# Kernel optimization log

Measured on AMD Instinct MI355X. Metric: run time of the kernel, lower is better.

## Reference

```python
import jax, jax.numpy as jnp
import numpy as np

N_NODES = 100000
IN_F = 256
OUT_F = 128
N_EDGES = 1600000


def setup_inputs() -> dict:
    key = jax.random.key(0)
    k1, k2, k3, k4, k5 = jax.random.split(key, 5)
    x = jax.random.normal(k1, (N_NODES, IN_F), dtype=jnp.float32)
    edge_index = jax.random.randint(k2, (2, N_EDGES), 0, N_NODES, dtype=jnp.int64)
    edge_weight = jax.random.uniform(k3, (N_EDGES,), dtype=jnp.float32)
    # Xavier-uniform init as in reset_parameters
    limit = float(np.sqrt(6.0 / (IN_F + OUT_F)))
    weight = jax.random.uniform(k4, (IN_F, OUT_F), dtype=jnp.float32,
                                minval=-limit, maxval=limit)
    return {"x": x, "edge_index": edge_index, "edge_weight": edge_weight,
            "weight": weight}


def reference(x, edge_index, edge_weight, weight):
    # support = X @ W  -- dense feature transform
    support = x @ weight                       # [N, out_f]
    # output = spmm(adj, support): out[dst] += w_e * support[src]
    dst = edge_index[0]
    src = edge_index[1]
    msgs = support[src] * edge_weight[:, None]  # [E, out_f] gather
    out = jax.ops.segment_sum(msgs, dst, num_segments=N_NODES)  # [N, out_f]
    return out
```

## Files before the change

### kernel.cpp

```cpp
#include <hip/hip_runtime.h>

#define N_NODES 100000
#define IN_F 256
#define OUT_F 128
#define NB 782
#define LCAP 4096

typedef float f32x4 __attribute__((ext_vector_type(4)));
typedef __bf16 bf16x8 __attribute__((ext_vector_type(8)));

__device__ inline unsigned cvt2_bf16(float a, float b) {
  unsigned ua = __float_as_uint(a), ub = __float_as_uint(b);
  ua = (ua + 0x7fffu + ((ua >> 16) & 1u)) >> 16;
  ub = (ub + 0x7fffu + ((ub >> 16) & 1u)) >> 16;
  return ua | (ub << 16);
}
__device__ inline unsigned short cvt1_bf16(float a) {
  unsigned ua = __float_as_uint(a);
  return (unsigned short)((ua + 0x7fffu + ((ua >> 16) & 1u)) >> 16);
}

__global__ __launch_bounds__(256) void transpose_w(const float* __restrict__ w,
                                                   uint4* __restrict__ wt) {
  int c = blockIdx.x * 256 + threadIdx.x;
  int l = c & 63;
  int kt = (c >> 6) & 7;
  int nt = c >> 9;
  int n = nt * 16 + (l & 15);
  int kb = kt * 32 + ((l >> 4) & 3) * 8;
  unsigned d[4];
#pragma unroll
  for (int j = 0; j < 4; ++j) {
    float a = w[(size_t)(kb + 2 * j) * OUT_F + n];
    float b = w[(size_t)(kb + 2 * j + 1) * OUT_F + n];
    d[j] = cvt2_bf16(a, b);
  }
  wt[c] = make_uint4(d[0], d[1], d[2], d[3]);
}

__global__ __launch_bounds__(256) void gemm_count(const float* __restrict__ x,
                                                  const uint4* __restrict__ wt,
                                                  unsigned short* __restrict__ sup,
                                                  const int* __restrict__ ei,
                                                  int* __restrict__ coarse,
                                                  int nedges, int nblk, int gblocks) {
  __shared__ uint4 As[1024];
  __shared__ uint4 Bs[1024];
  __shared__ int hist[NB];
  const int gid = blockIdx.x;
  const int t = threadIdx.x;

  int role, sub;
  int m = (gblocks < nblk) ? gblocks : nblk;
  if (gid < 2 * m) {
    role = gid & 1;
    sub = gid >> 1;
  } else if (nblk > gblocks) {
    role = 1;
    sub = gid - gblocks;
  } else {
    role = 0;
    sub = gid - nblk;
  }

  if (role == 1) {
    for (int i = t; i < NB; i += 256) hist[i] = 0;
    __syncthreads();
    const int base = sub * 2048;
#pragma unroll
    for (int j = 0; j < 8; ++j) {
      int e = base + j * 256 + t;
      if (e < nedges) atomicAdd(&hist[ei[e] >> 7], 1);
    }
    __syncthreads();
    for (int i = t; i < NB; i += 256) coarse[(size_t)sub * NB + i] = hist[i];
    return;
  }

  const int lane = t & 63;
  const int wv = t >> 6;
  const int wm = wv >> 1, wn = wv & 1;
  const int row0 = sub * 128;

  f32x4 acc[4][4];
#pragma unroll
  for (int mi = 0; mi < 4; ++mi)
#pragma unroll
    for (int ni = 0; ni < 4; ++ni) acc[mi][ni] = (f32x4){0.f, 0.f, 0.f, 0.f};

  for (int it = 0; it < 4; ++it) {
    const int k0 = it * 64;
#pragma unroll
    for (int i = 0; i < 4; ++i) {
      int ci = i * 256 + t;
      int g = ci >> 6, l = ci & 63;
      int mrow = (g >> 1) * 16 + (l & 15);
      int k = k0 + (g & 1) * 32 + ((l >> 4) & 3) * 8;
      int row = row0 + mrow;
      if (row > N_NODES - 1) row = N_NODES - 1;
      const float* src = x + (size_t)row * IN_F + k;
      f32x4 v0 = *(const f32x4*)src;
      f32x4 v1 = *(const f32x4*)(src + 4);
      As[ci] = make_uint4(cvt2_bf16(v0.x, v0.y), cvt2_bf16(v0.z, v0.w),
                          cvt2_bf16(v1.x, v1.y), cvt2_bf16(v1.z, v1.w));
      Bs[ci] = wt[((g >> 1) * 8 + it * 2 + (g & 1)) * 64 + l];
    }
    __syncthreads();
#pragma unroll
    for (int ktl = 0; ktl < 2; ++ktl) {
      bf16x8 af[4], bfr[4];
#pragma unroll
      for (int mi = 0; mi < 4; ++mi)
        af[mi] = *(bf16x8*)&As[((wm * 4 + mi) * 2 + ktl) * 64 + lane];
#pragma unroll
      for (int ni = 0; ni < 4; ++ni)
        bfr[ni] = *(bf16x8*)&Bs[((wn * 4 + ni) * 2 + ktl) * 64 + lane];
#pragma unroll
      for (int mi = 0; mi < 4; ++mi)
#pragma unroll
        for (int ni = 0; ni < 4; ++ni)
          acc[mi][ni] = __builtin_amdgcn_mfma_f32_16x16x32_bf16(af[mi], bfr[ni],
                                                                acc[mi][ni], 0, 0, 0);
    }
    __syncthreads();
  }

  const int quad = lane >> 4, col = lane & 15;
#pragma unroll
  for (int mi = 0; mi < 4; ++mi) {
#pragma unroll
    for (int r = 0; r < 4; ++r) {
      int row = row0 + (wm * 4 + mi) * 16 + quad * 4 + r;
      if (row < N_NODES) {
#pragma unroll
        for (int ni = 0; ni < 4; ++ni)
          sup[(size_t)row * OUT_F + (wn * 4 + ni) * 16 + col] =
              cvt1_bf16(acc[mi][ni][r]);
      }
    }
  }
}

__global__ __launch_bounds__(256) void colscan(int* __restrict__ coarse,
                                               int* __restrict__ coltot, int nblk) {
  __shared__ int s[256];
  const int bin = blockIdx.x;
  const int t = threadIdx.x;
  int carry = 0;
  for (int c0 = 0; c0 < nblk; c0 += 256) {
    int idx = c0 + t;
    int v = (idx < nblk) ? coarse[(size_t)idx * NB + bin] : 0;
    s[t] = v;
    __syncthreads();
    for (int off = 1; off < 256; off <<= 1) {
      int xv = (t >= off) ? s[t - off] : 0;
      __syncthreads();
      s[t] += xv;
      __syncthreads();
    }
    int excl = carry + ((t == 0) ? 0 : s[t - 1]);
    if (idx < nblk) coarse[(size_t)idx * NB + bin] = excl;
    carry += s[255];
    __syncthreads();
  }
  if (t == 0) coltot[bin] = carry;
}

__global__ __launch_bounds__(256) void scan1(int* __restrict__ a,
                                             int* __restrict__ bsum, int n) {
  __shared__ int s[256];
  const int t = threadIdx.x;
  const int base = blockIdx.x * 1024 + t * 4;
  int v0 = (base + 0 < n) ? a[base + 0] : 0;
  int v1 = (base + 1 < n) ? a[base + 1] : 0;
  int v2 = (base + 2 < n) ? a[base + 2] : 0;
  int v3 = (base + 3 < n) ? a[base + 3] : 0;
  v1 += v0; v2 += v1; v3 += v2;
  s[t] = v3;
  __syncthreads();
  for (int off = 1; off < 256; off <<= 1) {
    int xv = (t >= off) ? s[t - off] : 0;
    __syncthreads();
    s[t] += xv;
    __syncthreads();
  }
  int excl = (t == 0) ? 0 : s[t - 1];
  if (base + 0 < n) a[base + 0] = v0 + excl;
  if (base + 1 < n) a[base + 1] = v1 + excl;
  if (base + 2 < n) a[base + 2] = v2 + excl;
  if (base + 3 < n) a[base + 3] = v3 + excl;
  if (t == 255 && bsum) bsum[blockIdx.x] = s[255];
}

__global__ __launch_bounds__(256) void partition(const int* __restrict__ ei,
                                                 const float* __restrict__ ew,
                                                 const int* __restrict__ coarse,
                                                 const int* __restrict__ coltot,
                                                 int2* __restrict__ recs, int nedges) {
  __shared__ int wbase[NB];
  const int b = blockIdx.x;
  const int t = threadIdx.x;
  for (int i = t; i < NB; i += 256)
    wbase[i] = coarse[(size_t)b * NB + i] + (i ? coltot[i - 1] : 0);
  __syncthreads();
  const int base = b * 2048;
#pragma unroll
  for (int j = 0; j < 8; ++j) {
    int e = base + j * 256 + t;
    if (e < nedges) {
      int d = ei[e];
      int srcn = ei[nedges + e];
      float wv = ew[e];
      int bin = d >> 7;
      int pos = atomicAdd(&wbase[bin], 1);
      unsigned long long pk =
          (unsigned long long)(unsigned)((srcn << 7) | (d & 127)) |
          ((unsigned long long)__float_as_uint(wv) << 32);
      __builtin_nontemporal_store(pk, (unsigned long long*)&recs[pos]);
    }
  }
}

__global__ __launch_bounds__(256) void fine_csr(int2* __restrict__ recs,
                                                const int* __restrict__ coltot,
                                                int* __restrict__ rowptr) {
  __shared__ int2 lrec[LCAP];
  __shared__ int cnt[128];
  __shared__ int wp[128];
  const int bin = blockIdx.x;
  const int t = threadIdx.x;
  const int segStart = bin ? coltot[bin - 1] : 0;
  const int segEnd = coltot[bin];
  int nrec = segEnd - segStart;
  if (nrec > LCAP) nrec = LCAP;
  if (t < 128) cnt[t] = 0;
  __syncthreads();
  for (int i = t; i < nrec; i += 256) {
    int2 r = recs[segStart + i];
    lrec[i] = r;
    atomicAdd(&cnt[r.x & 127], 1);
  }
  __syncthreads();
  for (int off = 1; off < 128; off <<= 1) {
    int xv = (t >= off && t < 128) ? cnt[t - off] : 0;
    __syncthreads();
    if (t < 128) cnt[t] += xv;
    __syncthreads();
  }
  if (t < 128) {
    wp[t] = segStart + ((t == 0) ? 0 : cnt[t - 1]);
    int node = bin * 128 + t;
    if (node < N_NODES) rowptr[node + 1] = segStart + cnt[t];
  }
  if (bin == 0 && t == 0) rowptr[0] = 0;
  __syncthreads();
  for (int i = t; i < nrec; i += 256) {
    int2 r = lrec[i];
    int p = atomicAdd(&wp[r.x & 127], 1);
    recs[p] = make_int2(r.x >> 7, r.y);
  }
}

__global__ __launch_bounds__(256) void aggregate_bf16(const int* __restrict__ rowptr,
                                                      const int2* __restrict__ edges,
                                                      const unsigned short* __restrict__ sup,
                                                      float* __restrict__ out, int nnodes) {
  int wave = (int)((blockIdx.x * 256u + threadIdx.x) >> 6);
  int lane = threadIdx.x & 63;
  if (wave >= nnodes) return;
  int beg = rowptr[wave];
  int end = rowptr[wave + 1];
  float2 acc = make_float2(0.f, 0.f);
  int e = beg;
  for (; e + 4 <= end; e += 4) {
    int2 m0 = edges[e + 0];
    int2 m1 = edges[e + 1];
    int2 m2 = edges[e + 2];
    int2 m3 = edges[e + 3];
    unsigned u0 = *(const unsigned*)(sup + (size_t)m0.x * OUT_F + lane * 2);
    unsigned u1 = *(const unsigned*)(sup + (size_t)m1.x * OUT_F + lane * 2);
    unsigned u2 = *(const unsigned*)(sup + (size_t)m2.x * OUT_F + lane * 2);
    unsigned u3 = *(const unsigned*)(sup + (size_t)m3.x * OUT_F + lane * 2);
    float w0 = __int_as_float(m0.y), w1 = __int_as_float(m1.y);
    float w2 = __int_as_float(m2.y), w3 = __int_as_float(m3.y);
    acc.x = fmaf(__uint_as_float(u0 << 16), w0, acc.x);
    acc.y = fmaf(__uint_as_float(u0 & 0xffff0000u), w0, acc.y);
    acc.x = fmaf(__uint_as_float(u1 << 16), w1, acc.x);
    acc.y = fmaf(__uint_as_float(u1 & 0xffff0000u), w1, acc.y);
    acc.x = fmaf(__uint_as_float(u2 << 16), w2, acc.x);
    acc.y = fmaf(__uint_as_float(u2 & 0xffff0000u), w2, acc.y);
    acc.x = fmaf(__uint_as_float(u3 << 16), w3, acc.x);
    acc.y = fmaf(__uint_as_float(u3 & 0xffff0000u), w3, acc.y);
  }
  for (; e < end; ++e) {
    int2 m = edges[e];
    unsigned u = *(const unsigned*)(sup + (size_t)m.x * OUT_F + lane * 2);
    float w = __int_as_float(m.y);
    acc.x = fmaf(__uint_as_float(u << 16), w, acc.x);
    acc.y = fmaf(__uint_as_float(u & 0xffff0000u), w, acc.y);
  }
  *(float2*)(out + (size_t)wave * OUT_F + lane * 2) = acc;
}

__global__ __launch_bounds__(256) void gemm_mfma(const float* __restrict__ x,
                                                 const uint4* __restrict__ wt,
                                                 unsigned short* __restrict__ sup) {
  __shared__ uint4 As[1024];
  __shared__ uint4 Bs[1024];
  const int t = threadIdx.x;
  const int lane = t & 63;
  const int wv = t >> 6;
  const int wm = wv >> 1, wn = wv & 1;
  const int row0 = blockIdx.x * 128;

  f32x4 acc[4][4];
#pragma unroll
  for (int mi = 0; mi < 4; ++mi)
#pragma unroll
    for (int ni = 0; ni < 4; ++ni) acc[mi][ni] = (f32x4){0.f, 0.f, 0.f, 0.f};

  for (int it = 0; it < 4; ++it) {
    const int k0 = it * 64;
#pragma unroll
    for (int i = 0; i < 4; ++i) {
      int ci = i * 256 + t;
      int g = ci >> 6, l = ci & 63;
      int m = (g >> 1) * 16 + (l & 15);
      int k = k0 + (g & 1) * 32 + ((l >> 4) & 3) * 8;
      int row = row0 + m;
      if (row > N_NODES - 1) row = N_NODES - 1;
      const float* src = x + (size_t)row * IN_F + k;
      f32x4 v0 = *(const f32x4*)src;
      f32x4 v1 = *(const f32x4*)(src + 4);
      As[ci] = make_uint4(cvt2_bf16(v0.x, v0.y), cvt2_bf16(v0.z, v0.w),
                          cvt2_bf16(v1.x, v1.y), cvt2_bf16(v1.z, v1.w));
      Bs[ci] = wt[((g >> 1) * 8 + it * 2 + (g & 1)) * 64 + l];
    }
    __syncthreads();
#pragma unroll
    for (int ktl = 0; ktl < 2; ++ktl) {
      bf16x8 af[4], bfr[4];
#pragma unroll
      for (int mi = 0; mi < 4; ++mi)
        af[mi] = *(bf16x8*)&As[((wm * 4 + mi) * 2 + ktl) * 64 + lane];
#pragma unroll
      for (int ni = 0; ni < 4; ++ni)
        bfr[ni] = *(bf16x8*)&Bs[((wn * 4 + ni) * 2 + ktl) * 64 + lane];
#pragma unroll
      for (int mi = 0; mi < 4; ++mi)
#pragma unroll
        for (int ni = 0; ni < 4; ++ni)
          acc[mi][ni] = __builtin_amdgcn_mfma_f32_16x16x32_bf16(af[mi], bfr[ni],
                                                                acc[mi][ni], 0, 0, 0);
    }
    __syncthreads();
  }

  const int quad = lane >> 4, col = lane & 15;
#pragma unroll
  for (int mi = 0; mi < 4; ++mi) {
#pragma unroll
    for (int r = 0; r < 4; ++r) {
      int row = row0 + (wm * 4 + mi) * 16 + quad * 4 + r;
      if (row < N_NODES) {
#pragma unroll
        for (int ni = 0; ni < 4; ++ni)
          sup[(size_t)row * OUT_F + (wn * 4 + ni) * 16 + col] =
              cvt1_bf16(acc[mi][ni][r]);
      }
    }
  }
}

__global__ __launch_bounds__(256) void scatter_edges(const int* __restrict__ ei,
                                                     const float* __restrict__ ew,
                                                     const unsigned short* __restrict__ sup,
                                                     float* __restrict__ out, int nedges) {
  int gwave = (int)((blockIdx.x * 256u + threadIdx.x) >> 6);
  int lane = threadIdx.x & 63;
  if (gwave >= nedges) return;
  int dst = ei[gwave];
  int src = ei[nedges + gwave];
  float wgt = ew[gwave];
  unsigned u = *(const unsigned*)(sup + (size_t)src * OUT_F + lane * 2);
  float* op = out + (size_t)dst * OUT_F + lane * 2;
  atomicAdd(op, __uint_as_float(u << 16) * wgt);
  atomicAdd(op + 1, __uint_as_float(u & 0xffff0000u) * wgt);
}

extern "C" void kernel_launch(void* const* d_in, const int* in_sizes, int n_in,
                              void* d_out, int out_size, void* d_ws, size_t ws_size,
                              hipStream_t stream) {
  const float* x = (const float*)d_in[0];
  const int* ei = (const int*)d_in[1];
  const float* ew = (const float*)d_in[2];
  const float* w = (const float*)d_in[3];
  float* out = (float*)d_out;
  const int nedges = in_sizes[2];
  const int nblk = (nedges + 2047) / 2048;

  const size_t off_support = 0;
  const size_t sz_support = (size_t)N_NODES * OUT_F * 2;
  const size_t off_rowptr = off_support + sz_support;
  const size_t off_wt = off_rowptr + 400016;
  const size_t off_coltot = off_wt + 65536;
  const size_t off_coarse = off_coltot + 3136;
  const size_t sz_coarse = (size_t)nblk * NB * 4;
  const size_t off_recs = (off_coarse + sz_coarse + 15) & ~(size_t)15;
  const size_t total_ws = off_recs + (size_t)nedges * 8;

  unsigned short* support = (unsigned short*)((char*)d_ws + off_support);
  int* rowptr = (int*)((char*)d_ws + off_rowptr);
  uint4* wt = (uint4*)((char*)d_ws + off_wt);
  int* coltot = (int*)((char*)d_ws + off_coltot);
  int* coarse = (int*)((char*)d_ws + off_coarse);
  int2* recs = (int2*)((char*)d_ws + off_recs);

  transpose_w<<<16, 256, 0, stream>>>(w, wt);

  if (ws_size < total_ws) {
    const int gblocks = (N_NODES + 127) / 128;
    gemm_mfma<<<gblocks, 256, 0, stream>>>(x, wt, support);
    hipMemsetAsync(d_out, 0, (size_t)out_size * sizeof(float), stream);
    int sblocks = (nedges + 3) / 4;
    scatter_edges<<<sblocks, 256, 0, stream>>>(ei, ew, support, out, nedges);
    return;
  }

  const int gblocks = (N_NODES + 127) / 128;

  gemm_count<<<gblocks + nblk, 256, 0, stream>>>(x, wt, support, ei, coarse,
                                                 nedges, nblk, gblocks);
  colscan<<<NB, 256, 0, stream>>>(coarse, coltot, nblk);
  scan1<<<1, 256, 0, stream>>>(coltot, (int*)nullptr, NB);
  partition<<<nblk, 256, 0, stream>>>(ei, ew, coarse, coltot, recs, nedges);
  fine_csr<<<NB, 256, 0, stream>>>(recs, coltot, rowptr);

  const int ablocks = (N_NODES + 3) / 4;
  aggregate_bf16<<<ablocks, 256, 0, stream>>>(rowptr, recs, support, out, N_NODES);
}
```

Baseline: 350.8 us.

## Sort edges locally per block during GEMM, merge bins in fine CSR pass

The counting blocks that run alongside the GEMM now do a full local counting sort of their 2048 edges by coarse bin in shared memory. They write the sorted records and 16-bit per-block bin offsets to a workspace buffer. The separate partition kernel and the strided column scan are replaced by a simple per-bin column sum. The fine CSR kernel now gathers each bin's runs from every block buffer and sorts them through an index array instead of re-reading scattered records. This removes one full pass over the edge list and the random global scatter, at the cost of many small, poorly coalesced gathers in fine_csr2 and a lower per-bin capacity (3072).

```diff
diff --git a/kernel.cpp b/kernel.cpp
--- a/kernel.cpp
+++ b/kernel.cpp
@@ -4,7 +4,8 @@
 #define IN_F 256
 #define OUT_F 128
 #define NB 782
-#define LCAP 4096
+#define EPB 2048
+#define LCAP2 3072
 
 typedef float f32x4 __attribute__((ext_vector_type(4)));
 typedef __bf16 bf16x8 __attribute__((ext_vector_type(8)));
@@ -38,15 +39,15 @@
   wt[c] = make_uint4(d[0], d[1], d[2], d[3]);
 }
 
-__global__ __launch_bounds__(256) void gemm_count(const float* __restrict__ x,
-                                                  const uint4* __restrict__ wt,
-                                                  unsigned short* __restrict__ sup,
-                                                  const int* __restrict__ ei,
-                                                  int* __restrict__ coarse,
-                                                  int nedges, int nblk, int gblocks) {
-  __shared__ uint4 As[1024];
-  __shared__ uint4 Bs[1024];
-  __shared__ int hist[NB];
+__global__ __launch_bounds__(256) void gemm_sort(const float* __restrict__ x,
+                                                 const uint4* __restrict__ wt,
+                                                 unsigned short* __restrict__ sup,
+                                                 const int* __restrict__ ei,
+                                                 const float* __restrict__ ew,
+                                                 unsigned short* __restrict__ lst,
+                                                 int2* __restrict__ buf1,
+                                                 int nedges, int nblk, int gblocks) {
+  __shared__ __align__(16) char smem[32768];
   const int gid = blockIdx.x;
   const int t = threadIdx.x;
 
@@ -64,19 +65,63 @@
   }
 
   if (role == 1) {
+    int2* ebuf = (int2*)smem;
+    int* hist = (int*)(smem + 16384);
+    int* scn = (int*)(smem + 19520);
+    int* tmp = (int*)(smem + 22656);
+    const int base = sub * EPB;
+    const int nE = min(EPB, nedges - base);
+
     for (int i = t; i < NB; i += 256) hist[i] = 0;
     __syncthreads();
-    const int base = sub * 2048;
+    int d8[8], ok8[8];
 #pragma unroll
     for (int j = 0; j < 8; ++j) {
       int e = base + j * 256 + t;
-      if (e < nedges) atomicAdd(&hist[ei[e] >> 7], 1);
-    }
-    __syncthreads();
-    for (int i = t; i < NB; i += 256) coarse[(size_t)sub * NB + i] = hist[i];
+      ok8[j] = e < nedges;
+      d8[j] = ok8[j] ? ei[e] : 0;
+      if (ok8[j]) atomicAdd(&hist[d8[j] >> 7], 1);
+    }
+    __syncthreads();
+    int carry = 0;
+    for (int c0 = 0; c0 < NB; c0 += 256) {
+      int idx = c0 + t;
+      int v = (idx < NB) ? hist[idx] : 0;
+      tmp[t] = v;
+      __syncthreads();
+      for (int off = 1; off < 256; off <<= 1) {
+        int xv = (t >= off) ? tmp[t - off] : 0;
+        __syncthreads();
+        tmp[t] += xv;
+        __syncthreads();
+      }
+      if (idx < NB) scn[idx] = carry + tmp[t] - v;
+      int nc = carry + tmp[255];
+      __syncthreads();
+      carry = nc;
+    }
+    for (int i = t; i < NB; i += 256)
+      lst[(size_t)sub * (NB + 2) + i] = (unsigned short)scn[i];
+    if (t == 0) lst[(size_t)sub * (NB + 2) + NB] = (unsigned short)nE;
+    for (int i = t; i < NB; i += 256) hist[i] = scn[i];
+    __syncthreads();
+#pragma unroll
+    for (int j = 0; j < 8; ++j) {
+      if (ok8[j]) {
+        int e = base + j * 256 + t;
+        int srcn = ei[nedges + e];
+        float wv = ew[e];
+        int pos = atomicAdd(&hist[d8[j] >> 7], 1);
+        ebuf[pos] = make_int2((srcn << 7) | (d8[j] & 127), __float_as_int(wv));
+      }
+    }
+    __syncthreads();
+    for (int i = t; i < nE; i += 256) buf1[(size_t)sub * EPB + i] = ebuf[i];
     return;
   }
 
+  uint4* As = (uint4*)smem;
+  uint4* Bs = (uint4*)(smem + 16384);
   const int lane = t & 63;
   const int wv = t >> 6;
   const int wm = wv >> 1, wn = wv & 1;
@@ -141,29 +186,17 @@
   }
 }
 
-__global__ __launch_bounds__(256) void colscan(int* __restrict__ coarse,
-                                               int* __restrict__ coltot, int nblk) {
-  __shared__ int s[256];
-  const int bin = blockIdx.x;
-  const int t = threadIdx.x;
-  int carry = 0;
-  for (int c0 = 0; c0 < nblk; c0 += 256) {
-    int idx = c0 + t;
-    int v = (idx < nblk) ? coarse[(size_t)idx * NB + bin] : 0;
-    s[t] = v;
-    __syncthreads();
-    for (int off = 1; off < 256; off <<= 1) {
-      int xv = (t >= off) ? s[t - off] : 0;
-      __syncthreads();
-      s[t] += xv;
-      __syncthreads();
-    }
-    int excl = carry + ((t == 0) ? 0 : s[t - 1]);
-    if (idx < nblk) coarse[(size_t)idx * NB + bin] = excl;
-    carry += s[255];
-    __syncthreads();
-  }
-  if (t == 0) coltot[bin] = carry;
+__global__ __launch_bounds__(256) void colsum(const unsigned short* __restrict__ lst,
+                                              int* __restrict__ coltot, int nblk) {
+  int bin = blockIdx.x * 256 + threadIdx.x;
+  if (bin >= NB) return;
+  int sum = 0;
+  for (int s = 0; s < nblk; ++s) {
+    int a = lst[(size_t)s * (NB + 2) + bin];
+    int b = lst[(size_t)s * (NB + 2) + bin + 1];
+    sum += b - a;
+  }
+  coltot[bin] = sum;
 }
 
 __global__ __launch_bounds__(256) void scan1(int* __restrict__ a,
@@ -192,54 +225,57 @@
   if (t == 255 && bsum) bsum[blockIdx.x] = s[255];
 }
 
-__global__ __launch_bounds__(256) void partition(const int* __restrict__ ei,
-                                                 const float* __restrict__ ew,
-                                                 const int* __restrict__ coarse,
+__global__ __launch_bounds__(256) void fine_csr2(const int2* __restrict__ buf1,
+                                                 const unsigned short* __restrict__ lst,
                                                  const int* __restrict__ coltot,
-                                                 int2* __restrict__ recs, int nedges) {
-  __shared__ int wbase[NB];
-  const int b = blockIdx.x;
-  const int t = threadIdx.x;
-  for (int i = t; i < NB; i += 256)
-    wbase[i] = coarse[(size_t)b * NB + i] + (i ? coltot[i - 1] : 0);
-  __syncthreads();
-  const int base = b * 2048;
-#pragma unroll
-  for (int j = 0; j < 8; ++j) {
-    int e = base + j * 256 + t;
-    if (e < nedges) {
-      int d = ei[e];
-      int srcn = ei[nedges + e];
-      float wv = ew[e];
-      int bin = d >> 7;
-      int pos = atomicAdd(&wbase[bin], 1);
-      unsigned long long pk =
-          (unsigned long long)(unsigned)((srcn << 7) | (d & 127)) |
-          ((unsigned long long)__float_as_uint(wv) << 32);
-      __builtin_nontemporal_store(pk, (unsigned long long*)&recs[pos]);
-    }
-  }
-}
-
-__global__ __launch_bounds__(256) void fine_csr(int2* __restrict__ recs,
-                                                const int* __restrict__ coltot,
-                                                int* __restrict__ rowptr) {
-  __shared__ int2 lrec[LCAP];
-  __shared__ int cnt[128];
-  __shared__ int wp[128];
+                                                 int2* __restrict__ recs,
+                                                 int* __restrict__ rowptr, int nblk) {
+  __shared__ int2 stg[LCAP2];
+  __shared__ unsigned short sidx[LCAP2];
+  __shared__ unsigned short aoff[800];
+  __shared__ int soff[800];
+  __shared__ int tmp[256];
+  __shared__ int cnt[128], wp[128];
   const int bin = blockIdx.x;
   const int t = threadIdx.x;
-  const int segStart = bin ? coltot[bin - 1] : 0;
-  const int segEnd = coltot[bin];
-  int nrec = segEnd - segStart;
-  if (nrec > LCAP) nrec = LCAP;
+
+  int carry = 0;
+  for (int c0 = 0; c0 < nblk; c0 += 256) {
+    int s = c0 + t;
+    int a = 0, b = 0;
+    if (s < nblk) {
+      a = lst[(size_t)s * (NB + 2) + bin];
+      b = lst[(size_t)s * (NB + 2) + bin + 1];
+      aoff[s] = (unsigned short)a;
+    }
+    int v = b - a;
+    tmp[t] = v;
+    __syncthreads();
+    for (int off = 1; off < 256; off <<= 1) {
+      int xv = (t >= off) ? tmp[t - off] : 0;
+      __syncthreads();
+      tmp[t] += xv;
+      __syncthreads();
+    }
+    if (s < nblk) soff[s] = carry + tmp[t] - v;
+    int nc = carry + tmp[255];
+    __syncthreads();
+    carry = nc;
+  }
+  int nrec = carry;
+  if (nrec > LCAP2) nrec = LCAP2;
+  for (int s = t; s < nblk; s += 256) {
+    int o = soff[s];
+    int a = aoff[s];
+    int l = (((s + 1) < nblk) ? soff[s + 1] : carry) - o;
+    for (int k = 0; k < l; ++k) {
+      int q = o + k;
+      if (q < LCAP2) stg[q] = buf1[(size_t)s * EPB + a + k];
+    }
+  }
   if (t < 128) cnt[t] = 0;
   __syncthreads();
-  for (int i = t; i < nrec; i += 256) {
-    int2 r = recs[segStart + i];
-    lrec[i] = r;
-    atomicAdd(&cnt[r.x & 127], 1);
-  }
+  for (int i = t; i < nrec; i += 256) atomicAdd(&cnt[stg[i].x & 127], 1);
   __syncthreads();
   for (int off = 1; off < 128; off <<= 1) {
     int xv = (t >= off && t < 128) ? cnt[t - off] : 0;
@@ -247,17 +283,22 @@
     if (t < 128) cnt[t] += xv;
     __syncthreads();
   }
+  const int segStart = bin ? coltot[bin - 1] : 0;
   if (t < 128) {
-    wp[t] = segStart + ((t == 0) ? 0 : cnt[t - 1]);
+    wp[t] = (t == 0) ? 0 : cnt[t - 1];
     int node = bin * 128 + t;
     if (node < N_NODES) rowptr[node + 1] = segStart + cnt[t];
   }
   if (bin == 0 && t == 0) rowptr[0] = 0;
   __syncthreads();
   for (int i = t; i < nrec; i += 256) {
-    int2 r = lrec[i];
-    int p = atomicAdd(&wp[r.x & 127], 1);
-    recs[p] = make_int2(r.x >> 7, r.y);
+    int p = atomicAdd(&wp[stg[i].x & 127], 1);
+    sidx[p] = (unsigned short)i;
+  }
+  __syncthreads();
+  for (int q = t; q < nrec; q += 256) {
+    int2 r = stg[sidx[q]];
+    recs[segStart + q] = make_int2(r.x >> 7, r.y);
   }
 }
 
@@ -397,28 +438,31 @@
   const float* w = (const float*)d_in[3];
   float* out = (float*)d_out;
   const int nedges = in_sizes[2];
-  const int nblk = (nedges + 2047) / 2048;
+  const int nblk = (nedges + EPB - 1) / EPB;
 
   const size_t off_support = 0;
   const size_t sz_support = (size_t)N_NODES * OUT_F * 2;
   const size_t off_rowptr = off_support + sz_support;
   const size_t off_wt = off_rowptr + 400016;
   const size_t off_coltot = off_wt + 65536;
-  const size_t off_coarse = off_coltot + 3136;
-  const size_t sz_coarse = (size_t)nblk * NB * 4;
-  const size_t off_recs = (off_coarse + sz_coarse + 15) & ~(size_t)15;
+  const size_t off_lst = off_coltot + 3152;
+  const size_t sz_lst = (size_t)nblk * (NB + 2) * 2;
+  const size_t off_buf1 = (off_lst + sz_lst + 15) & ~(size_t)15;
+  const size_t sz_buf1 = (size_t)nblk * EPB * 8;
+  const size_t off_recs = off_buf1 + sz_buf1;
   const size_t total_ws = off_recs + (size_t)nedges * 8;
 
   unsigned short* support = (unsigned short*)((char*)d_ws + off_support);
   int* rowptr = (int*)((char*)d_ws + off_rowptr);
   uint4* wt = (uint4*)((char*)d_ws + off_wt);
   int* coltot = (int*)((char*)d_ws + off_coltot);
-  int* coarse = (int*)((char*)d_ws + off_coarse);
+  unsigned short* lst = (unsigned short*)((char*)d_ws + off_lst);
+  int2* buf1 = (int2*)((char*)d_ws + off_buf1);
   int2* recs = (int2*)((char*)d_ws + off_recs);
 
   transpose_w<<<16, 256, 0, stream>>>(w, wt);
 
-  if (ws_size < total_ws) {
+  if (ws_size < total_ws || nblk > 800) {
     const int gblocks = (N_NODES + 127) / 128;
     gemm_mfma<<<gblocks, 256, 0, stream>>>(x, wt, support);
     hipMemsetAsync(d_out, 0, (size_t)out_size * sizeof(float), stream);
@@ -429,12 +473,11 @@
 
   const int gblocks = (N_NODES + 127) / 128;
 
-  gemm_count<<<gblocks + nblk, 256, 0, stream>>>(x, wt, support, ei, coarse,
-                                                 nedges, nblk, gblocks);
-  colscan<<<NB, 256, 0, stream>>>(coarse, coltot, nblk);
+  gemm_sort<<<gblocks + nblk, 256, 0, stream>>>(x, wt, support, ei, ew, lst,
+                                                buf1, nedges, nblk, gblocks);
+  colsum<<<(NB + 255) / 256, 256, 0, stream>>>(lst, coltot, nblk);
   scan1<<<1, 256, 0, stream>>>(coltot, (int*)nullptr, NB);
-  partition<<<nblk, 256, 0, stream>>>(ei, ew, coarse, coltot, recs, nedges);
-  fine_csr<<<NB, 256, 0, stream>>>(recs, coltot, rowptr);
+  fine_csr2<<<NB, 256, 0, stream>>>(buf1, lst, coltot, recs, rowptr, nblk);
 
   const int ablocks = (N_NODES + 3) / 4;
   aggregate_bf16<<<ablocks, 256, 0, stream>>>(rowptr, recs, support, out, N_NODES);
```

After: 409.9 us. +16.8%, slower.
